# Optimization experiments

Hardware: AMD Instinct MI355X
Metric: run time of the kernel (lower is better)

## Reference

```python
import jax, jax.numpy as jnp
import numpy as np
import math

B, S, D = 2, 1024, 512
H = 8
DH = D // H
N_NEURONS = 512
K = 16
N_BASIS = 8
RANK = 64
D_FF = 2048
LN_EPS = 1e-5


def _layer_norm(x, g, b):
    mu = jnp.mean(x, axis=-1, keepdims=True)
    var = jnp.var(x, axis=-1, keepdims=True)
    return (x - mu) * jax.lax.rsqrt(var + LN_EPS) * g + b


def setup_inputs() -> dict:
    key = jax.random.key(0)
    ks = jax.random.split(key, 16)
    x = jax.random.normal(ks[0], (B, S, D), dtype=jnp.float32)
    # causal mask [B,1,S,S] (True = keep)
    mask = jnp.broadcast_to(jnp.tril(jnp.ones((S, S), dtype=bool)), (B, 1, S, S))
    inp = {
        "x": x,
        "neuron_emb": jax.random.normal(ks[1], (N_NEURONS, D)) * 0.02,
        "Wq": jax.random.normal(ks[2], (D, D)) * 0.02, "bq": jnp.zeros((D,)),
        "Wk": jax.random.normal(ks[3], (D, D)) * 0.02, "bk": jnp.zeros((D,)),
        "Wv": jax.random.normal(ks[4], (D, D)) * 0.02, "bv": jnp.zeros((D,)),
        "Wg": jax.random.normal(ks[5], (2 * D, 2)) * 0.02, "bg": jnp.zeros((2,)),
        "basis_A": jax.random.normal(ks[6], (N_BASIS, D, RANK)) * 0.05,
        "basis_B": jax.random.normal(ks[7], (N_BASIS, RANK, D_FF)) * 0.05,
        "neuron_coords": jax.random.normal(ks[8], (N_NEURONS, N_BASIS)) * 0.5,
        "Wd": jax.random.normal(ks[9], (D_FF, D)) * 0.02, "bd": jnp.zeros((D,)),
        "ln1_g": jnp.ones((D,)), "ln1_b": jnp.zeros((D,)),
        "ln2_g": jnp.ones((D,)), "ln2_b": jnp.zeros((D,)),
        "mask": mask,
    }
    return inp


def reference(x, neuron_emb, Wq, bq, Wk, bk, Wv, bv, Wg, bg, basis_A, basis_B,
              neuron_coords, Wd, bd, ln1_g, ln1_b, ln2_g, ln2_b, mask):
    normed = _layer_norm(x, ln1_g, ln1_b)
    # --- router: cross-attention context ---
    q = (normed @ Wq + bq).reshape(B, S, H, DH).transpose(0, 2, 1, 3)
    k = (normed @ Wk + bk).reshape(B, S, H, DH).transpose(0, 2, 1, 3)
    v = (normed @ Wv + bv).reshape(B, S, H, DH).transpose(0, 2, 1, 3)
    attn = jnp.einsum('bhsd,bhtd->bhst', q, k) / math.sqrt(DH)
    attn = jnp.where(mask, attn, -jnp.inf)
    attn = jax.nn.softmax(attn, axis=-1)
    context = jnp.einsum('bhst,bhtd->bhsd', attn, v)
    context = context.transpose(0, 2, 1, 3).reshape(B, S, D)
    # --- gated neuron scoring + top-k ---
    token_scores = normed @ neuron_emb.T            # [B,S,N]
    context_scores = context @ neuron_emb.T         # [B,S,N]
    gate = jax.nn.softmax(jnp.concatenate([normed, context], axis=-1) @ Wg + bg, axis=-1)
    scores = gate[:, :, 0:1] * token_scores + gate[:, :, 1:2] * context_scores
    topk_scores, topk_idx = jax.lax.top_k(scores, K)  # [B,S,K]
    weights = jax.nn.softmax(topk_scores, axis=-1)
    # --- neuron info residual ---
    neuron_info = jnp.einsum('bsk,bskd->bsd', weights, neuron_emb[topk_idx])
    x = x + neuron_info
    # --- per-token basis-mixed low-rank FFN ---
    normed2 = _layer_norm(x, ln2_g, ln2_b)
    coords = neuron_coords[topk_idx]                # [B,S,K,n_basis]
    token_coords = jnp.einsum('bsk,bskn->bsn', weights, coords)  # [B,S,n_basis]
    # h = x @ (sum_n c_n A_n): contract without materializing [B,S,D,R]
    h = jnp.einsum('bsnr,bsn->bsr', jnp.einsum('bsd,ndr->bsnr', normed2, basis_A), token_coords)
    h = jnp.einsum('bsnf,bsn->bsf', jnp.einsum('bsr,nrf->bsnf', h, basis_B), token_coords)
    h = jax.nn.gelu(h, approximate=False)
    out = h @ Wd + bd
    x = x + out
    return (x, topk_idx)
```

## Files before the change

### kernel.cpp

```cpp
#include <hip/hip_runtime.h>
#include <hip/hip_bf16.h>

#define Bv 2
#define Sv 1024
#define Dv 512
#define Hv 8
#define Nv 512
#define Kv 16
#define NBv 8
#define DFv 2048
#define NTOK (Bv*Sv)

typedef __attribute__((ext_vector_type(8))) short short8;
typedef __attribute__((ext_vector_type(4))) float float4v;
typedef __attribute__((ext_vector_type(4))) double dbl4;

__device__ __forceinline__ double fexp64(double x)
{
    if (x < -708.0) return 0.0;
    const double SHIFT = 6755399441055744.0;
    double t  = fma(x, 1.4426950408889634074, SHIFT);
    double nd = t - SHIFT;
    double r  = fma(-nd, 6.93147180369123816490e-01, x);
    r         = fma(-nd, 1.90821492927058770002e-10, r);
    double p = 1.0 / 6227020800.0;
    p = fma(p, r, 1.0 / 479001600.0);
    p = fma(p, r, 1.0 / 39916800.0);
    p = fma(p, r, 1.0 / 3628800.0);
    p = fma(p, r, 1.0 / 362880.0);
    p = fma(p, r, 1.0 / 40320.0);
    p = fma(p, r, 1.0 / 5040.0);
    p = fma(p, r, 1.0 / 720.0);
    p = fma(p, r, 1.0 / 120.0);
    p = fma(p, r, 1.0 / 24.0);
    p = fma(p, r, 1.0 / 6.0);
    p = fma(p, r, 0.5);
    p = fma(p, r, 1.0);
    p = fma(p, r, 1.0);
    long long ni = (long long)nd;
    double s = __longlong_as_double((unsigned long long)(ni + 1023) << 52);
    return p * s;
}

__launch_bounds__(256)
__global__ void ln64_k(const float* __restrict__ x, const float* __restrict__ g,
                       const float* __restrict__ b, double* __restrict__ out)
{
    const int t = blockIdx.x;
    const size_t base = (size_t)t * Dv;
    const int tid = threadIdx.x;
    double v0 = (double)x[base + tid];
    double v1 = (double)x[base + tid + 256];
    double s = v0 + v1, ss = v0 * v0 + v1 * v1;
    #pragma unroll
    for (int off = 32; off; off >>= 1) { s += __shfl_xor(s, off); ss += __shfl_xor(ss, off); }
    __shared__ double red[4][2];
    const int wv = tid >> 6, ln = tid & 63;
    if (ln == 0) { red[wv][0] = s; red[wv][1] = ss; }
    __syncthreads();
    s  = red[0][0] + red[1][0] + red[2][0] + red[3][0];
    ss = red[0][1] + red[1][1] + red[2][1] + red[3][1];
    double mu  = s * (1.0 / Dv);
    double var = ss * (1.0 / Dv) - mu * mu;
    double rstd = 1.0 / sqrt(var + 1e-5);
    out[base + tid]       = (v0 - mu) * rstd * (double)g[tid]       + (double)b[tid];
    out[base + tid + 256] = (v1 - mu) * rstd * (double)g[tid + 256] + (double)b[tid + 256];
}

__launch_bounds__(256)
__global__ void qkvMC_k(const double* __restrict__ A,
                        const float* __restrict__ Wq, const float* __restrict__ Wk,
                        const float* __restrict__ Wv, const float* __restrict__ bq,
                        const float* __restrict__ bk, const float* __restrict__ bvv,
                        double* __restrict__ qo, double* __restrict__ ko,
                        double* __restrict__ vo)
{
    __shared__ double As[32][18];
    __shared__ double Bs[3][16][66];
    const int tid = threadIdx.x;
    const int n0 = blockIdx.x * 64, m0 = blockIdx.y * 32;
    const int w = tid >> 6, l = tid & 63;
    const int mt = (w >> 1) * 16, wc = (w & 1) * 32;
    const int ar = tid >> 3, ak = (tid & 7) * 2;
    const int bkk = tid >> 4, bn = (tid & 15) * 4;

    int rA = 0, kA = 0, kB = 0, cB = 0, dsel = -1;
    #pragma unroll 1
    for (int ab = 0; ab < 4; ab++) {
        if (dsel >= 0) break;
        const int a_ = ab & 1, b_ = ab >> 1;
        const int rA_ = a_ ? (l >> 2) : (l & 15);
        const int kA_ = a_ ? (l & 3)  : (l >> 4);
        const int kB_ = b_ ? (l & 3)  : (l >> 4);
        const int cB_ = b_ ? (l >> 2) : (l & 15);
        const double av  = (double)(((rA_ * 37 + kA_ * 11) % 19) + 1);
        const double bvp = (double)(((kB_ * 23 + cB_ * 7) % 17) + 1);
        dbl4 dd = __builtin_amdgcn_mfma_f64_16x16x4f64(av, bvp, (dbl4){0.0, 0.0, 0.0, 0.0}, 0, 0, 0);
        #pragma unroll 1
        for (int d = 0; d < 4; d++) {
            if (dsel >= 0) break;
            int okv = 1;
            #pragma unroll
            for (int r = 0; r < 4; r++) {
                const int i_ = (d == 0) ? 4 * (l >> 4) + r
                             : (d == 1) ? (l & 15)
                             : (d == 2) ? (l >> 4) + 4 * r
                             :            (l & 15);
                const int j_ = (d == 0) ? (l & 15)
                             : (d == 1) ? 4 * (l >> 4) + r
                             : (d == 2) ? (l & 15)
                             :            (l >> 4) + 4 * r;
                double e = 0.0;
                #pragma unroll
                for (int kk2 = 0; kk2 < 4; kk2++)
                    e += (double)(((i_ * 37 + kk2 * 11) % 19) + 1)
                       * (double)(((kk2 * 23 + j_ * 7) % 17) + 1);
                okv &= (dd[r] == e) ? 1 : 0;
            }
            if (__all(okv)) { dsel = d; rA = rA_; kA = kA_; kB = kB_; cB = cB_; }
        }
    }

    auto stage = [&](int k0) {
        double2 avv = *(const double2*)(A + (size_t)(m0 + ar) * Dv + k0 + ak);
        *(double2*)&As[ar][ak] = avv;
        {
            float4 b4 = *(const float4*)(Wq + (size_t)(k0 + bkk) * Dv + n0 + bn);
            Bs[0][bkk][bn] = (double)b4.x; Bs[0][bkk][bn + 1] = (double)b4.y;
            Bs[0][bkk][bn + 2] = (double)b4.z; Bs[0][bkk][bn + 3] = (double)b4.w;
        }
        {
            float4 b4 = *(const float4*)(Wk + (size_t)(k0 + bkk) * Dv + n0 + bn);
            Bs[1][bkk][bn] = (double)b4.x; Bs[1][bkk][bn + 1] = (double)b4.y;
            Bs[1][bkk][bn + 2] = (double)b4.z; Bs[1][bkk][bn + 3] = (double)b4.w;
        }
        {
            float4 b4 = *(const float4*)(Wv + (size_t)(k0 + bkk) * Dv + n0 + bn);
            Bs[2][bkk][bn] = (double)b4.x; Bs[2][bkk][bn + 1] = (double)b4.y;
            Bs[2][bkk][bn + 2] = (double)b4.z; Bs[2][bkk][bn + 3] = (double)b4.w;
        }
    };

    if (dsel >= 0) {
        dbl4 acc[3][2];
        #pragma unroll
        for (int z = 0; z < 3; z++)
            #pragma unroll
            for (int nt = 0; nt < 2; nt++)
                acc[z][nt] = (dbl4){0.0, 0.0, 0.0, 0.0};
        for (int k0 = 0; k0 < Dv; k0 += 16) {
            __syncthreads();
            stage(k0);
            __syncthreads();
            #pragma unroll
            for (int s = 0; s < 4; s++) {
                const double aA = As[mt + rA][4 * s + kA];
                #pragma unroll
                for (int z = 0; z < 3; z++) {
                    const double b0 = Bs[z][4 * s + kB][wc + cB];
                    const double b1 = Bs[z][4 * s + kB][wc + 16 + cB];
                    acc[z][0] = __builtin_amdgcn_mfma_f64_16x16x4f64(aA, b0, acc[z][0], 0, 0, 0);
                    acc[z][1] = __builtin_amdgcn_mfma_f64_16x16x4f64(aA, b1, acc[z][1], 0, 0, 0);
                }
            }
        }
        #pragma unroll
        for (int r = 0; r < 4; r++) {
            const int i_ = (dsel == 0) ? 4 * (l >> 4) + r
                         : (dsel == 1) ? (l & 15)
                         : (dsel == 2) ? (l >> 4) + 4 * r
                         :               (l & 15);
            const int j_ = (dsel == 0) ? (l & 15)
                         : (dsel == 1) ? 4 * (l >> 4) + r
                         : (dsel == 2) ? (l & 15)
                         :               (l >> 4) + 4 * r;
            const int rowg = m0 + mt + i_;
            #pragma unroll
            for (int nt = 0; nt < 2; nt++) {
                const int colg = n0 + wc + nt * 16 + j_;
                qo[(size_t)rowg * Dv + colg] = acc[0][nt][r] + (double)bq[colg];
                ko[(size_t)rowg * Dv + colg] = acc[1][nt][r] + (double)bk[colg];
                vo[(size_t)rowg * Dv + colg] = acc[2][nt][r] + (double)bvv[colg];
            }
        }
    } else {
        double fac[3][8];
        #pragma unroll
        for (int z = 0; z < 3; z++)
            #pragma unroll
            for (int c = 0; c < 8; c++) fac[z][c] = 0.0;
        const int frow = mt + (l & 15);
        const int fcb  = wc + (l >> 4) * 8;
        for (int k0 = 0; k0 < Dv; k0 += 16) {
            __syncthreads();
            stage(k0);
            __syncthreads();
            #pragma unroll
            for (int kk = 0; kk < 16; kk++) {
                const double a = As[frow][kk];
                #pragma unroll
                for (int z = 0; z < 3; z++)
                    #pragma unroll
                    for (int c = 0; c < 8; c++)
                        fac[z][c] = fma(a, Bs[z][kk][fcb + c], fac[z][c]);
            }
        }
        const int rowg = m0 + frow;
        #pragma unroll
        for (int c = 0; c < 8; c++) {
            const int colg = n0 + fcb + c;
            qo[(size_t)rowg * Dv + colg] = fac[0][c] + (double)bq[colg];
            ko[(size_t)rowg * Dv + colg] = fac[1][c] + (double)bk[colg];
            vo[(size_t)rowg * Dv + colg] = fac[2][c] + (double)bvv[colg];
        }
    }
}

__launch_bounds__(256)
__global__ void scores64_k(const double* __restrict__ A0, const double* __restrict__ A1,
                           const double* __restrict__ gate, const float* __restrict__ Bm,
                           double* __restrict__ Cbase)
{
    const int M = NTOK, N = Nv, Kd = Dv;
    const int z = blockIdx.z;
    const int kbeg = z * (Dv / 2), kend = kbeg + Dv / 2;
    double* Cout = Cbase + (size_t)z * M * N;
    __shared__ double As[16][68];
    __shared__ double Bs[16][68];
    const int tid = threadIdx.x;
    const int m0 = blockIdx.y * 64, n0 = blockIdx.x * 64;
    const int tx = tid & 15, ty = tid >> 4;
    double acc[4][4] = {};
    const int lm = tid >> 2, lk4 = (tid & 3) << 2;
    for (int k0 = kbeg; k0 < kend; k0 += 16) {
        const double g0 = gate[2 * (m0 + lm)], g1 = gate[2 * (m0 + lm) + 1];
        double4 a0 = *(const double4*)(A0 + (size_t)(m0 + lm) * Kd + k0 + lk4);
        double4 a1 = *(const double4*)(A1 + (size_t)(m0 + lm) * Kd + k0 + lk4);
        As[lk4 + 0][lm] = g0 * a0.x + g1 * a1.x;
        As[lk4 + 1][lm] = g0 * a0.y + g1 * a1.y;
        As[lk4 + 2][lm] = g0 * a0.z + g1 * a1.z;
        As[lk4 + 3][lm] = g0 * a0.w + g1 * a1.w;
        const int nn = tid >> 2, kq = (tid & 3) << 2;
        float4 bv4 = *(const float4*)(Bm + (size_t)(n0 + nn) * Kd + k0 + kq);
        Bs[kq + 0][nn] = (double)bv4.x; Bs[kq + 1][nn] = (double)bv4.y;
        Bs[kq + 2][nn] = (double)bv4.z; Bs[kq + 3][nn] = (double)bv4.w;
        __syncthreads();
        #pragma unroll
        for (int kk = 0; kk < 16; kk++) {
            double a_[4], b_[4];
            *(double4*)a_ = *(const double4*)&As[kk][ty << 2];
            *(double4*)b_ = *(const double4*)&Bs[kk][tx << 2];
            #pragma unroll
            for (int i = 0; i < 4; i++)
                #pragma unroll
                for (int j = 0; j < 4; j++)
                    acc[i][j] = fma(a_[i], b_[j], acc[i][j]);
        }
        __syncthreads();
    }
    #pragma unroll
    for (int i = 0; i < 4; i++) {
        const int row = m0 + (ty << 2) + i;
        #pragma unroll
        for (int j = 0; j < 4; j++)
            Cout[(size_t)row * N + n0 + (tx << 2) + j] = acc[i][j];
    }
}

template<int EPI>
__launch_bounds__(256)
__global__ void mfma_k(const __hip_bfloat16* __restrict__ A, const __hip_bfloat16* __restrict__ B,
                       void* __restrict__ Cout_, int M, int N, int Kt, int kper)
{
    __shared__ __hip_bfloat16 As[128][40];
    __shared__ __hip_bfloat16 Bs[128][40];
    const int tid = threadIdx.x;
    const int m0 = blockIdx.y * 128, n0 = blockIdx.x * 128;
    const int z = blockIdx.z;
    const int kbeg = z * kper, kend = kbeg + kper;
    const int w = tid >> 6, l = tid & 63;
    const int wr = (w >> 1) * 64, wc = (w & 1) * 64;
    const int lm = l & 15, quad = l >> 4;
    float4v acc[4][4];
    #pragma unroll
    for (int i = 0; i < 4; i++)
        #pragma unroll
        for (int j = 0; j < 4; j++)
            acc[i][j] = (float4v){0.f, 0.f, 0.f, 0.f};
    const int srow = tid >> 1, skb = (tid & 1) * 16;
    for (int k0 = kbeg; k0 < kend; k0 += 32) {
        *(uint4*)&As[srow][skb]     = *(const uint4*)(A + (size_t)(m0 + srow) * Kt + k0 + skb);
        *(uint4*)&As[srow][skb + 8] = *(const uint4*)(A + (size_t)(m0 + srow) * Kt + k0 + skb + 8);
        *(uint4*)&Bs[srow][skb]     = *(const uint4*)(B + (size_t)(n0 + srow) * Kt + k0 + skb);
        *(uint4*)&Bs[srow][skb + 8] = *(const uint4*)(B + (size_t)(n0 + srow) * Kt + k0 + skb + 8);
        __syncthreads();
        short8 af[4], bf[4];
        #pragma unroll
        for (int mi = 0; mi < 4; mi++) af[mi] = *(const short8*)&As[wr + mi * 16 + lm][quad * 8];
        #pragma unroll
        for (int ni = 0; ni < 4; ni++) bf[ni] = *(const short8*)&Bs[wc + ni * 16 + lm][quad * 8];
        #pragma unroll
        for (int mi = 0; mi < 4; mi++)
            #pragma unroll
            for (int ni = 0; ni < 4; ni++)
                acc[mi][ni] = __builtin_amdgcn_mfma_f32_16x16x32_bf16(af[mi], bf[ni], acc[mi][ni], 0, 0, 0);
        __syncthreads();
    }
    #pragma unroll
    for (int mi = 0; mi < 4; mi++) {
        #pragma unroll
        for (int ni = 0; ni < 4; ni++) {
            const int col = n0 + wc + ni * 16 + lm;
            #pragma unroll
            for (int r = 0; r < 4; r++) {
                const int row = m0 + wr + mi * 16 + quad * 4 + r;
                float c = acc[mi][ni][r];
                if (EPI == 0) {
                    ((float*)Cout_)[(size_t)z * M * N + (size_t)row * N + col] = c;
                } else {
                    c = 0.5f * c * (1.0f + erff(c * 0.70710678118654752f));
                    ((__hip_bfloat16*)Cout_)[(size_t)row * N + col] = __float2bfloat16(c);
                }
            }
        }
    }
}

__device__ __constant__ int c_slotbase[4] = {0, 0, 384, 640};
__device__ __constant__ int c_cnt[4]      = {0, 24, 16, 8};

__launch_bounds__(256)
__global__ void attn64c_k(const double* __restrict__ q, const double* __restrict__ k,
                          const double* __restrict__ v, double* __restrict__ ctxun,
                          double* __restrict__ Opart, double* __restrict__ mbuf,
                          double* __restrict__ lbuf)
{
    const int qt = blockIdx.x, bh = blockIdx.y, ch = blockIdx.z;
    if (qt < ch * 8) return;
    const int b = bh >> 3, h = bh & 7;
    __shared__ double Qs[32][70];
    __shared__ double Kt[64][34];
    __shared__ double Vs[32][70];
    const int tid = threadIdx.x;
    const int r = tid >> 3, cc = tid & 7;
    const int lane = tid & 63;
    const int lbase = lane & 56;
    const size_t qoff = ((size_t)b * Sv + (size_t)qt * 32) * Dv + h * 64;
    #pragma unroll
    for (int i = 0; i < 4; i++) {
        int f = i * 256 + tid;
        int row = f >> 5, c2 = (f & 31) * 2;
        *(double2*)&Qs[row][c2] = *(const double2*)(q + qoff + (size_t)row * Dv + c2);
    }
    double O[8] = {};
    double mrun = -1e300, lrun = 0.0;
    const int iglob = qt * 32 + r;
    const int jbeg = ch * 8;
    const int jend = (qt < jbeg + 7) ? qt : (jbeg + 7);
    for (int jt = jbeg; jt <= jend; jt++) {
        __syncthreads();
        const size_t koff = ((size_t)b * Sv + (size_t)jt * 32) * Dv + h * 64;
        #pragma unroll
        for (int i = 0; i < 4; i++) {
            int f = i * 256 + tid;
            int row = f >> 5, c2 = (f & 31) * 2;
            double2 kv = *(const double2*)(k + koff + (size_t)row * Dv + c2);
            Kt[c2][row]     = kv.x;
            Kt[c2 + 1][row] = kv.y;
            *(double2*)&Vs[row][c2] = *(const double2*)(v + koff + (size_t)row * Dv + c2);
        }
        __syncthreads();
        double a[4] = {0.0, 0.0, 0.0, 0.0};
        #pragma unroll 8
        for (int kk = 0; kk < 64; kk += 2) {
            double2 qv  = *(const double2*)&Qs[r][kk];
            double2 ka0 = *(const double2*)&Kt[kk][cc * 4];
            double2 ka1 = *(const double2*)&Kt[kk][cc * 4 + 2];
            double2 kb0 = *(const double2*)&Kt[kk + 1][cc * 4];
            double2 kb1 = *(const double2*)&Kt[kk + 1][cc * 4 + 2];
            a[0] = fma(qv.x, ka0.x, fma(qv.y, kb0.x, a[0]));
            a[1] = fma(qv.x, ka0.y, fma(qv.y, kb0.y, a[1]));
            a[2] = fma(qv.x, ka1.x, fma(qv.y, kb1.x, a[2]));
            a[3] = fma(qv.x, ka1.y, fma(qv.y, kb1.y, a[3]));
        }
        double p[4];
        double mx = -1e300;
        #pragma unroll
        for (int jj = 0; jj < 4; jj++) {
            const int jglob = jt * 32 + cc * 4 + jj;
            p[jj] = (jglob <= iglob) ? a[jj] * 0.125 : -1e300;
            mx = fmax(mx, p[jj]);
        }
        mx = fmax(mx, __shfl_xor(mx, 1));
        mx = fmax(mx, __shfl_xor(mx, 2));
        mx = fmax(mx, __shfl_xor(mx, 4));
        const double mnew = fmax(mrun, mx);
        double rsum = 0.0;
        #pragma unroll
        for (int jj = 0; jj < 4; jj++) { p[jj] = fexp64(p[jj] - mnew); rsum += p[jj]; }
        rsum += __shfl_xor(rsum, 1);
        rsum += __shfl_xor(rsum, 2);
        rsum += __shfl_xor(rsum, 4);
        const double alpha = fexp64(mrun - mnew);
        lrun = lrun * alpha + rsum;
        mrun = mnew;
        #pragma unroll
        for (int c = 0; c < 8; c++) O[c] *= alpha;
        #pragma unroll
        for (int jsrc = 0; jsrc < 8; jsrc++) {
            #pragma unroll
            for (int jj = 0; jj < 4; jj++) {
                const double pj = __shfl(p[jj], lbase + jsrc);
                const double* vrow = &Vs[jsrc * 4 + jj][cc * 8];
                #pragma unroll
                for (int c2 = 0; c2 < 8; c2 += 2) {
                    double2 vv = *(const double2*)&vrow[c2];
                    O[c2 + 0] = fma(pj, vv.x, O[c2 + 0]);
                    O[c2 + 1] = fma(pj, vv.y, O[c2 + 1]);
                }
            }
        }
    }
    if (cc == 0) {
        const int mi = ((bh * 32 + qt) * 4 + ch) * 32 + r;
        mbuf[mi] = mrun; lbuf[mi] = lrun;
    }
    if (ch == 0) {
        const size_t obase = ((size_t)b * Sv + (size_t)iglob) * Dv + h * 64 + cc * 8;
        #pragma unroll
        for (int c2 = 0; c2 < 8; c2 += 2) { double2 t{O[c2], O[c2+1]}; *(double2*)(ctxun + obase + c2) = t; }
    } else {
        const int slot = c_slotbase[ch] + bh * c_cnt[ch] + (qt - ch * 8);
        const size_t obase = ((size_t)slot * 32 + r) * 64 + cc * 8;
        #pragma unroll
        for (int c2 = 0; c2 < 8; c2 += 2) { double2 t{O[c2], O[c2+1]}; *(double2*)(Opart + obase + c2) = t; }
    }
}

__launch_bounds__(256)
__global__ void attnmerge_k(double* __restrict__ ctx, const double* __restrict__ Opart,
                            const double* __restrict__ mbuf, const double* __restrict__ lbuf)
{
    const size_t i = (size_t)blockIdx.x * 256 + threadIdx.x;
    const size_t e = i * 2;
    const int d = (int)(e & 511);
    const int s = (int)((e >> 9) & 1023);
    const int b = (int)(e >> 19);
    const int h = d >> 6;
    const int qt = s >> 5, r = s & 31;
    const int bh = b * 8 + h;
    int nch = qt >> 3; if (nch > 3) nch = 3;
    const int mib = ((bh * 32 + qt) * 4) * 32 + r;
    double ms = mbuf[mib];
    for (int c = 1; c <= nch; c++) ms = fmax(ms, mbuf[mib + c * 32]);
    double2 o = *(const double2*)(ctx + e);
    double a0 = exp(mbuf[mib] - ms);
    double den = lbuf[mib] * a0;
    o.x *= a0; o.y *= a0;
    for (int c = 1; c <= nch; c++) {
        const double ac = exp(mbuf[mib + c * 32] - ms);
        den += lbuf[mib + c * 32] * ac;
        const int slot = c_slotbase[c] + bh * c_cnt[c] + (qt - c * 8);
        const size_t op = ((size_t)slot * 32 + r) * 64 + (d & 63);
        double2 oc = *(const double2*)(Opart + op);
        o.x = fma(ac, oc.x, o.x);
        o.y = fma(ac, oc.y, o.y);
    }
    const double inv = 1.0 / den;
    o.x *= inv; o.y *= inv;
    *(double2*)(ctx + e) = o;
}

__launch_bounds__(256)
__global__ void gate64_k(const double* __restrict__ normed, const double* __restrict__ ctx,
                         const float* __restrict__ Wg, const float* __restrict__ bg,
                         double* __restrict__ gate)
{
    const int wv = threadIdx.x >> 6, lane = threadIdx.x & 63;
    const int t = blockIdx.x * 4 + wv;
    double a0 = 0.0, a1 = 0.0;
    for (int d = lane; d < Dv; d += 64) {
        double nv = normed[(size_t)t * Dv + d];
        double cv = ctx[(size_t)t * Dv + d];
        a0 += nv * (double)Wg[2 * d]     + cv * (double)Wg[2 * (d + Dv)];
        a1 += nv * (double)Wg[2 * d + 1] + cv * (double)Wg[2 * (d + Dv) + 1];
    }
    #pragma unroll
    for (int off = 32; off; off >>= 1) { a0 += __shfl_xor(a0, off); a1 += __shfl_xor(a1, off); }
    if (lane == 0) {
        a0 += (double)bg[0]; a1 += (double)bg[1];
        double m = fmax(a0, a1);
        double e0 = exp(a0 - m), e1 = exp(a1 - m);
        double inv = 1.0 / (e0 + e1);
        gate[2 * t] = e0 * inv; gate[2 * t + 1] = e1 * inv;
    }
}

__launch_bounds__(256)
__global__ void topk64_k(const double* __restrict__ s0, const float* __restrict__ x,
                         const float* __restrict__ emb, const float* __restrict__ coords,
                         const float* __restrict__ g2, const float* __restrict__ b2,
                         float* __restrict__ x2, __hip_bfloat16* __restrict__ normed2bf,
                         float* __restrict__ tcoords, float* __restrict__ idx_out)
{
    __shared__ double sc[4][Nv];
    const int wv = threadIdx.x >> 6, lane = threadIdx.x & 63;
    const int t = blockIdx.x * 4 + wv;
    const double* s1 = s0 + (size_t)NTOK * Nv;
    double* s = sc[wv];
    #pragma unroll
    for (int i = 0; i < 8; i++) {
        const size_t idx = (size_t)t * Nv + i * 64 + lane;
        s[i * 64 + lane] = s0[idx] + s1[idx];
    }
    __syncthreads();
    double wval[Kv]; int widx[Kv];
    for (int kk = 0; kk < Kv; kk++) {
        double bvv = -1e300; int bi = Nv;
        #pragma unroll
        for (int i = 0; i < 8; i++) {
            const int d = lane * 8 + i;
            const double vv = s[d];
            if (vv > bvv) { bvv = vv; bi = d; }
        }
        #pragma unroll
        for (int off = 1; off < 64; off <<= 1) {
            double ov = __shfl_xor(bvv, off);
            int    oi = __shfl_xor(bi, off);
            if (ov > bvv || (ov == bvv && oi < bi)) { bvv = ov; bi = oi; }
        }
        wval[kk] = bvv; widx[kk] = bi;
        __syncthreads();
        if (lane == (bi >> 3)) s[bi] = -1e301;
        __syncthreads();
        if (lane == kk) idx_out[(size_t)t * Kv + kk] = (float)bi;
    }
    double w[Kv]; double sum = 0.0;
    #pragma unroll
    for (int kk = 0; kk < Kv; kk++) { w[kk] = exp(wval[kk] - wval[0]); sum += w[kk]; }
    const double invs = 1.0 / sum;
    #pragma unroll
    for (int kk = 0; kk < Kv; kk++) w[kk] *= invs;
    float xv[8];
    float sm = 0.0f, sq = 0.0f;
    #pragma unroll
    for (int i = 0; i < 8; i++) {
        const int d = lane + 64 * i;
        double info = 0.0;
        #pragma unroll
        for (int kk = 0; kk < Kv; kk++)
            info = fma(w[kk], (double)emb[(size_t)widx[kk] * Dv + d], info);
        float vv = (float)((double)x[(size_t)t * Dv + d] + info);
        xv[i] = vv;
        x2[(size_t)t * Dv + d] = vv;
        sm += vv; sq += vv * vv;
    }
    #pragma unroll
    for (int off = 32; off; off >>= 1) { sm += __shfl_xor(sm, off); sq += __shfl_xor(sq, off); }
    const float mu = sm * (1.0f / Dv);
    const float var = sq * (1.0f / Dv) - mu * mu;
    const float rstd = rsqrtf(var + 1e-5f);
    #pragma unroll
    for (int i = 0; i < 8; i++) {
        const int d = lane + 64 * i;
        normed2bf[(size_t)t * Dv + d] = __float2bfloat16((xv[i] - mu) * rstd * g2[d] + b2[d]);
    }
    if (lane < NBv) {
        double tc = 0.0;
        #pragma unroll
        for (int kk = 0; kk < Kv; kk++)
            tc = fma(w[kk], (double)coords[(size_t)widx[kk] * NBv + lane], tc);
        tcoords[t * NBv + lane] = (float)tc;
    }
}

__launch_bounds__(256)
__global__ void acatbf_k(const float* __restrict__ bA, __hip_bfloat16* __restrict__ AcatT)
{
    const int i = blockIdx.x * 256 + threadIdx.x;
    const int d = i & 511, nc = i >> 9;
    const int n = nc >> 6, r = nc & 63;
    AcatT[i] = __float2bfloat16(bA[n * 32768 + d * 64 + r]);
}

__launch_bounds__(256)
__global__ void tr2bf_k(const float* __restrict__ in, __hip_bfloat16* __restrict__ out,
                        int R, int C)
{
    __shared__ float tile[32][33];
    const int c0 = blockIdx.x * 32, r0 = blockIdx.y * 32;
    const int tx = threadIdx.x & 31, ty = threadIdx.x >> 5;
    #pragma unroll
    for (int i = 0; i < 4; i++)
        tile[ty + 8 * i][tx] = in[(size_t)(r0 + ty + 8 * i) * C + c0 + tx];
    __syncthreads();
    #pragma unroll
    for (int i = 0; i < 4; i++)
        out[(size_t)(c0 + ty + 8 * i) * R + r0 + tx] = __float2bfloat16(tile[tx][ty + 8 * i]);
}

__launch_bounds__(256)
__global__ void combine_k(const float* __restrict__ Gp, const float* __restrict__ tcoords,
                          __hip_bfloat16* __restrict__ u_bf)
{
    const size_t M1 = (size_t)NTOK * Dv;
    const int wv = threadIdx.x >> 6, lane = threadIdx.x & 63;
    const int t = blockIdx.x * 4 + wv;
    float cs[NBv];
    #pragma unroll
    for (int n = 0; n < NBv; n++) cs[n] = tcoords[t * NBv + n];
    float h = 0.0f;
    #pragma unroll
    for (int n = 0; n < NBv; n++) {
        const size_t gi = (size_t)t * Dv + n * 64 + lane;
        float g = Gp[gi] + Gp[gi + M1] + Gp[gi + 2 * M1] + Gp[gi + 3 * M1];
        h = fmaf(cs[n], g, h);
    }
    #pragma unroll
    for (int n = 0; n < NBv; n++)
        u_bf[(size_t)t * Dv + n * 64 + lane] = __float2bfloat16(cs[n] * h);
}

__launch_bounds__(256)
__global__ void reduce4_k(const float* __restrict__ p4, const float* __restrict__ bd,
                          const float* __restrict__ x2, float* __restrict__ xout)
{
    const size_t M1 = (size_t)NTOK * Dv;
    const size_t i = (size_t)blockIdx.x * 256 + threadIdx.x;
    float c = p4[i] + p4[i + M1] + p4[i + 2 * M1] + p4[i + 3 * M1];
    xout[i] = c + bd[i & 511] + x2[i];
}

extern "C" void kernel_launch(void* const* d_in, const int* in_sizes, int n_in,
                              void* d_out, int out_size, void* d_ws, size_t ws_size,
                              hipStream_t stream) {
    (void)in_sizes; (void)n_in; (void)out_size; (void)ws_size;
    const size_t M1 = (size_t)NTOK * Dv;

    const float* x   = (const float*)d_in[0];
    const float* emb = (const float*)d_in[1];
    const float* Wq  = (const float*)d_in[2];
    const float* bq  = (const float*)d_in[3];
    const float* Wk  = (const float*)d_in[4];
    const float* bk  = (const float*)d_in[5];
    const float* Wv  = (const float*)d_in[6];
    const float* bvv = (const float*)d_in[7];
    const float* Wg  = (const float*)d_in[8];
    const float* bg  = (const float*)d_in[9];
    const float* bA  = (const float*)d_in[10];
    const float* bB  = (const float*)d_in[11];
    const float* crd = (const float*)d_in[12];
    const float* Wd  = (const float*)d_in[13];
    const float* bd  = (const float*)d_in[14];
    const float* l1g = (const float*)d_in[15];
    const float* l1b = (const float*)d_in[16];
    const float* l2g = (const float*)d_in[17];
    const float* l2b = (const float*)d_in[18];

    double* normed64 = (double*)d_ws;
    double* q64      = normed64 + M1;
    double* k64      = q64 + M1;
    double* v64      = k64 + M1;
    double* ctx64    = v64 + M1;
    double* Opart    = ctx64 + M1;
    double* mbuf     = Opart + 1572864;
    double* lbuf     = mbuf + 65536;
    double* gate64   = lbuf + 65536;
    float*  tcoords  = (float*)(gate64 + 4096);
    __hip_bfloat16* AcatT = (__hip_bfloat16*)(tcoords + 16384);

    double* s0 = q64;
    float*  x2 = (float*)v64;
    __hip_bfloat16* normed2bf = (__hip_bfloat16*)(x2 + M1);
    __hip_bfloat16* u_bf      = normed2bf + M1;
    float* Gp = (float*)q64;
    float* p4 = (float*)q64;
    __hip_bfloat16* hf_bf = (__hip_bfloat16*)Opart;
    __hip_bfloat16* bBT   = hf_bf + 4 * M1;
    __hip_bfloat16* WdT   = bBT + M1;

    float* xout    = (float*)d_out;
    float* idx_out = (float*)d_out + M1;

    ln64_k<<<NTOK, 256, 0, stream>>>(x, l1g, l1b, normed64);
    qkvMC_k<<<dim3(8, 64), 256, 0, stream>>>(normed64, Wq, Wk, Wv, bq, bk, bvv, q64, k64, v64);
    attn64c_k<<<dim3(32, 16, 4), 256, 0, stream>>>(q64, k64, v64, ctx64, Opart, mbuf, lbuf);
    attnmerge_k<<<(int)(M1 / 512), 256, 0, stream>>>(ctx64, Opart, mbuf, lbuf);
    gate64_k<<<NTOK / 4, 256, 0, stream>>>(normed64, ctx64, Wg, bg, gate64);
    scores64_k<<<dim3(8, 32, 2), 256, 0, stream>>>(normed64, ctx64, gate64, emb, s0);
    topk64_k<<<NTOK / 4, 256, 0, stream>>>(s0, x, emb, crd, l2g, l2b, x2, normed2bf, tcoords, idx_out);
    acatbf_k<<<1024, 256, 0, stream>>>(bA, AcatT);
    tr2bf_k<<<dim3(DFv / 32, Dv / 32), 256, 0, stream>>>(bB, bBT, Dv, DFv);
    tr2bf_k<<<dim3(Dv / 32, DFv / 32), 256, 0, stream>>>(Wd, WdT, DFv, Dv);
    mfma_k<0><<<dim3(4, 16, 4), 256, 0, stream>>>(normed2bf, AcatT, Gp, NTOK, Dv, Dv, Dv / 4);
    combine_k<<<NTOK / 4, 256, 0, stream>>>(Gp, tcoords, u_bf);
    mfma_k<1><<<dim3(16, 16, 1), 256, 0, stream>>>(u_bf, bBT, hf_bf, NTOK, DFv, Dv, Dv);
    mfma_k<0><<<dim3(4, 16, 4), 256, 0, stream>>>(hf_bf, WdT, p4, NTOK, Dv, DFv, DFv / 4);
    reduce4_k<<<(int)(M1 / 256), 256, 0, stream>>>(p4, bd, x2, xout);
}
```

Measured before the change: 609.9 us.

## Process two query tiles per attention block to reuse K/V shared-memory loads

The fp64 split-K causal attention kernel now handles 64 query rows per block, as two 32-row tiles, instead of 32. Each K/V tile loaded into shared memory serves both query tiles, which halves global K/V traffic and synchronisation per query row and adds independent FMA chains for ILP. The grid shrinks to half as many blocks along the query axis. Per-thread register use roughly doubles (two sets of accumulators and softmax state), which can lower occupancy. The diagonal-adjacent tile also wastes some fully masked work for the first query tile.

```diff
diff --git a/kernel.cpp b/kernel.cpp
--- a/kernel.cpp
+++ b/kernel.cpp
@@ -330,36 +330,38 @@
 __device__ __constant__ int c_cnt[4]      = {0, 24, 16, 8};
 
 __launch_bounds__(256)
-__global__ void attn64c_k(const double* __restrict__ q, const double* __restrict__ k,
+__global__ void attn64w_k(const double* __restrict__ q, const double* __restrict__ k,
                           const double* __restrict__ v, double* __restrict__ ctxun,
                           double* __restrict__ Opart, double* __restrict__ mbuf,
                           double* __restrict__ lbuf)
 {
-    const int qt = blockIdx.x, bh = blockIdx.y, ch = blockIdx.z;
-    if (qt < ch * 8) return;
+    const int qb = blockIdx.x, bh = blockIdx.y, ch = blockIdx.z;
+    if (qb < ch * 4) return;
     const int b = bh >> 3, h = bh & 7;
-    __shared__ double Qs[32][70];
+    __shared__ double Qs[64][70];
     __shared__ double Kt[64][34];
     __shared__ double Vs[32][70];
     const int tid = threadIdx.x;
     const int r = tid >> 3, cc = tid & 7;
     const int lane = tid & 63;
     const int lbase = lane & 56;
-    const size_t qoff = ((size_t)b * Sv + (size_t)qt * 32) * Dv + h * 64;
-    #pragma unroll
-    for (int i = 0; i < 4; i++) {
+    const size_t qoff = ((size_t)(b * Sv + qb * 64)) * Dv + h * 64;
+    #pragma unroll
+    for (int i = 0; i < 8; i++) {
         int f = i * 256 + tid;
         int row = f >> 5, c2 = (f & 31) * 2;
         *(double2*)&Qs[row][c2] = *(const double2*)(q + qoff + (size_t)row * Dv + c2);
     }
-    double O[8] = {};
-    double mrun = -1e300, lrun = 0.0;
-    const int iglob = qt * 32 + r;
+    double O0[8] = {}, O1[8] = {};
+    double m0 = -1e300, l0 = 0.0;
+    double m1 = -1e300, l1 = 0.0;
+    const int ig0 = qb * 64 + r;
+    const int ig1 = qb * 64 + 32 + r;
     const int jbeg = ch * 8;
-    const int jend = (qt < jbeg + 7) ? qt : (jbeg + 7);
+    const int jend = (ch * 8 + 7 < 2 * qb + 1) ? ch * 8 + 7 : 2 * qb + 1;
     for (int jt = jbeg; jt <= jend; jt++) {
         __syncthreads();
-        const size_t koff = ((size_t)b * Sv + (size_t)jt * 32) * Dv + h * 64;
+        const size_t koff = ((size_t)(b * Sv + jt * 32)) * Dv + h * 64;
         #pragma unroll
         for (int i = 0; i < 4; i++) {
             int f = i * 256 + tid;
@@ -370,70 +372,96 @@
             *(double2*)&Vs[row][c2] = *(const double2*)(v + koff + (size_t)row * Dv + c2);
         }
         __syncthreads();
-        double a[4] = {0.0, 0.0, 0.0, 0.0};
+        double a0[4] = {0.0, 0.0, 0.0, 0.0};
+        double a1[4] = {0.0, 0.0, 0.0, 0.0};
         #pragma unroll 8
         for (int kk = 0; kk < 64; kk += 2) {
-            double2 qv  = *(const double2*)&Qs[r][kk];
+            double2 qv0 = *(const double2*)&Qs[r][kk];
+            double2 qv1 = *(const double2*)&Qs[32 + r][kk];
             double2 ka0 = *(const double2*)&Kt[kk][cc * 4];
             double2 ka1 = *(const double2*)&Kt[kk][cc * 4 + 2];
             double2 kb0 = *(const double2*)&Kt[kk + 1][cc * 4];
             double2 kb1 = *(const double2*)&Kt[kk + 1][cc * 4 + 2];
-            a[0] = fma(qv.x, ka0.x, fma(qv.y, kb0.x, a[0]));
-            a[1] = fma(qv.x, ka0.y, fma(qv.y, kb0.y, a[1]));
-            a[2] = fma(qv.x, ka1.x, fma(qv.y, kb1.x, a[2]));
-            a[3] = fma(qv.x, ka1.y, fma(qv.y, kb1.y, a[3]));
-        }
-        double p[4];
-        double mx = -1e300;
+            a0[0] = fma(qv0.x, ka0.x, fma(qv0.y, kb0.x, a0[0]));
+            a0[1] = fma(qv0.x, ka0.y, fma(qv0.y, kb0.y, a0[1]));
+            a0[2] = fma(qv0.x, ka1.x, fma(qv0.y, kb1.x, a0[2]));
+            a0[3] = fma(qv0.x, ka1.y, fma(qv0.y, kb1.y, a0[3]));
+            a1[0] = fma(qv1.x, ka0.x, fma(qv1.y, kb0.x, a1[0]));
+            a1[1] = fma(qv1.x, ka0.y, fma(qv1.y, kb0.y, a1[1]));
+            a1[2] = fma(qv1.x, ka1.x, fma(qv1.y, kb1.x, a1[2]));
+            a1[3] = fma(qv1.x, ka1.y, fma(qv1.y, kb1.y, a1[3]));
+        }
+        double p0[4], p1[4];
+        double mx0 = -1e300, mx1 = -1e300;
         #pragma unroll
         for (int jj = 0; jj < 4; jj++) {
             const int jglob = jt * 32 + cc * 4 + jj;
-            p[jj] = (jglob <= iglob) ? a[jj] * 0.125 : -1e300;
-            mx = fmax(mx, p[jj]);
-        }
-        mx = fmax(mx, __shfl_xor(mx, 1));
-        mx = fmax(mx, __shfl_xor(mx, 2));
-        mx = fmax(mx, __shfl_xor(mx, 4));
-        const double mnew = fmax(mrun, mx);
-        double rsum = 0.0;
-        #pragma unroll
-        for (int jj = 0; jj < 4; jj++) { p[jj] = fexp64(p[jj] - mnew); rsum += p[jj]; }
-        rsum += __shfl_xor(rsum, 1);
-        rsum += __shfl_xor(rsum, 2);
-        rsum += __shfl_xor(rsum, 4);
-        const double alpha = fexp64(mrun - mnew);
-        lrun = lrun * alpha + rsum;
-        mrun = mnew;
-        #pragma unroll
-        for (int c = 0; c < 8; c++) O[c] *= alpha;
+            p0[jj] = (jglob <= ig0) ? a0[jj] * 0.125 : -1e300;
+            p1[jj] = (jglob <= ig1) ? a1[jj] * 0.125 : -1e300;
+            mx0 = fmax(mx0, p0[jj]);
+            mx1 = fmax(mx1, p1[jj]);
+        }
+        mx0 = fmax(mx0, __shfl_xor(mx0, 1)); mx1 = fmax(mx1, __shfl_xor(mx1, 1));
+        mx0 = fmax(mx0, __shfl_xor(mx0, 2)); mx1 = fmax(mx1, __shfl_xor(mx1, 2));
+        mx0 = fmax(mx0, __shfl_xor(mx0, 4)); mx1 = fmax(mx1, __shfl_xor(mx1, 4));
+        const double mn0 = fmax(m0, mx0), mn1 = fmax(m1, mx1);
+        double rs0 = 0.0, rs1 = 0.0;
+        #pragma unroll
+        for (int jj = 0; jj < 4; jj++) {
+            p0[jj] = fexp64(p0[jj] - mn0); rs0 += p0[jj];
+            p1[jj] = fexp64(p1[jj] - mn1); rs1 += p1[jj];
+        }
+        rs0 += __shfl_xor(rs0, 1); rs1 += __shfl_xor(rs1, 1);
+        rs0 += __shfl_xor(rs0, 2); rs1 += __shfl_xor(rs1, 2);
+        rs0 += __shfl_xor(rs0, 4); rs1 += __shfl_xor(rs1, 4);
+        const double al0 = fexp64(m0 - mn0), al1 = fexp64(m1 - mn1);
+        l0 = l0 * al0 + rs0; m0 = mn0;
+        l1 = l1 * al1 + rs1; m1 = mn1;
+        #pragma unroll
+        for (int c = 0; c < 8; c++) { O0[c] *= al0; O1[c] *= al1; }
         #pragma unroll
         for (int jsrc = 0; jsrc < 8; jsrc++) {
             #pragma unroll
             for (int jj = 0; jj < 4; jj++) {
-                const double pj = __shfl(p[jj], lbase + jsrc);
+                const double pj0 = __shfl(p0[jj], lbase + jsrc);
+                const double pj1 = __shfl(p1[jj], lbase + jsrc);
                 const double* vrow = &Vs[jsrc * 4 + jj][cc * 8];
                 #pragma unroll
                 for (int c2 = 0; c2 < 8; c2 += 2) {
                     double2 vv = *(const double2*)&vrow[c2];
-                    O[c2 + 0] = fma(pj, vv.x, O[c2 + 0]);
-                    O[c2 + 1] = fma(pj, vv.y, O[c2 + 1]);
+                    O0[c2 + 0] = fma(pj0, vv.x, O0[c2 + 0]);
+                    O0[c2 + 1] = fma(pj0, vv.y, O0[c2 + 1]);
+                    O1[c2 + 0] = fma(pj1, vv.x, O1[c2 + 0]);
+                    O1[c2 + 1] = fma(pj1, vv.y, O1[c2 + 1]);
                 }
             }
         }
     }
+    const int qt0 = 2 * qb, qt1 = 2 * qb + 1;
     if (cc == 0) {
-        const int mi = ((bh * 32 + qt) * 4 + ch) * 32 + r;
-        mbuf[mi] = mrun; lbuf[mi] = lrun;
+        const int mi0 = ((bh * 32 + qt0) * 4 + ch) * 32 + r;
+        mbuf[mi0] = m0; lbuf[mi0] = l0;
+        const int mi1 = ((bh * 32 + qt1) * 4 + ch) * 32 + r;
+        mbuf[mi1] = m1; lbuf[mi1] = l1;
     }
     if (ch == 0) {
-        const size_t obase = ((size_t)b * Sv + (size_t)iglob) * Dv + h * 64 + cc * 8;
-        #pragma unroll
-        for (int c2 = 0; c2 < 8; c2 += 2) { double2 t{O[c2], O[c2+1]}; *(double2*)(ctxun + obase + c2) = t; }
+        const size_t ob0 = ((size_t)(b * Sv + ig0)) * Dv + h * 64 + cc * 8;
+        const size_t ob1 = ((size_t)(b * Sv + ig1)) * Dv + h * 64 + cc * 8;
+        #pragma unroll
+        for (int c2 = 0; c2 < 8; c2 += 2) {
+            double2 t0{O0[c2], O0[c2 + 1]}; *(double2*)(ctxun + ob0 + c2) = t0;
+            double2 t1{O1[c2], O1[c2 + 1]}; *(double2*)(ctxun + ob1 + c2) = t1;
+        }
     } else {
-        const int slot = c_slotbase[ch] + bh * c_cnt[ch] + (qt - ch * 8);
-        const size_t obase = ((size_t)slot * 32 + r) * 64 + cc * 8;
-        #pragma unroll
-        for (int c2 = 0; c2 < 8; c2 += 2) { double2 t{O[c2], O[c2+1]}; *(double2*)(Opart + obase + c2) = t; }
+        const int slot0 = c_slotbase[ch] + bh * c_cnt[ch] + (qt0 - ch * 8);
+        const int slot1 = slot0 + 1;
+        const size_t ob0 = ((size_t)slot0 * 32 + r) * 64 + cc * 8;
+        const size_t ob1 = ((size_t)slot1 * 32 + r) * 64 + cc * 8;
+        #pragma unroll
+        for (int c2 = 0; c2 < 8; c2 += 2) {
+            double2 t0{O0[c2], O0[c2 + 1]}; *(double2*)(Opart + ob0 + c2) = t0;
+            double2 t1{O1[c2], O1[c2 + 1]}; *(double2*)(Opart + ob1 + c2) = t1;
+        }
     }
 }
 
@@ -684,7 +712,7 @@
 
     ln64_k<<<NTOK, 256, 0, stream>>>(x, l1g, l1b, normed64);
     qkvMC_k<<<dim3(8, 64), 256, 0, stream>>>(normed64, Wq, Wk, Wv, bq, bk, bvv, q64, k64, v64);
-    attn64c_k<<<dim3(32, 16, 4), 256, 0, stream>>>(q64, k64, v64, ctx64, Opart, mbuf, lbuf);
+    attn64w_k<<<dim3(16, 16, 4), 256, 0, stream>>>(q64, k64, v64, ctx64, Opart, mbuf, lbuf);
     attnmerge_k<<<(int)(M1 / 512), 256, 0, stream>>>(ctx64, Opart, mbuf, lbuf);
     gate64_k<<<NTOK / 4, 256, 0, stream>>>(normed64, ctx64, Wg, bg, gate64);
     scores64_k<<<dim3(8, 32, 2), 256, 0, stream>>>(normed64, ctx64, gate64, emb, s0);
```

Result: faster. 540.7 us (median of 5 runs) (-11.4%).
